# Optimization experiments

Hardware: AMD Instinct MI355X
Metric: run time of the kernel (lower is better)

The kernel has to match this reference:

```python
import jax, jax.numpy as jnp
import numpy as np

B, O, I, D = 8, 128, 128, 1024


def setup_inputs() -> dict:
    key = jax.random.key(0)
    ks = jax.random.split(key, 10)
    s = 1.0 / np.sqrt(2 * D)  # torch Linear default-ish scale
    return {
        "output": jax.random.normal(ks[0], (B, O, D), jnp.float32),
        "context": jax.random.normal(ks[1], (B, I, D), jnp.float32),
        "mask": jax.random.randint(ks[2], (B, I), 0, 2, jnp.int32),
        # self.w = Linear(2*dim, dim), split into the output-half and context-half
        "w_out_w": jax.random.normal(ks[3], (D, D), jnp.float32) * s,
        "w_ctx_w": jax.random.normal(ks[4], (D, D), jnp.float32) * s,
        "w_b": jax.random.normal(ks[5], (D,), jnp.float32) * s,
        # self.score = Linear(dim, 1)
        "score_w": jax.random.normal(ks[6], (D,), jnp.float32) * (1.0 / np.sqrt(D)),
        "score_b": jnp.zeros((), jnp.float32),
        # self.linear_out = Linear(2*dim, dim)
        "lin_w": jax.random.normal(ks[7], (2 * D, D), jnp.float32) * s,
        "lin_b": jax.random.normal(ks[8], (D,), jnp.float32) * s,
    }


def reference(output, context, mask, w_out_w, w_ctx_w, w_b, score_w, score_b, lin_w, lin_b):
    # Additive (Bahdanau) attention.
    # cat(out, ctx) @ W^T == out @ W1 + ctx @ W2  -> avoid [B,O,I,2D] concat.
    s_out = jnp.einsum('bod,de->boe', output, w_out_w)            # [B,O,D]
    s_ctx = jnp.einsum('bid,de->bie', context, w_ctx_w)           # [B,I,D]
    h = jax.nn.leaky_relu(s_out[:, :, None, :] + s_ctx[:, None, :, :] + w_b)  # [B,O,I,D]
    score = jnp.einsum('boid,d->boi', h, score_w) + score_b       # [B,O,I]
    score = jnp.where(mask[:, None, :] == 1, -jnp.inf, score)
    attn = jax.nn.softmax(score, axis=-1)                         # [B,O,I]
    attn_output = jnp.einsum('boi,bid->bod', attn, context)       # mix=True: bmm
    # fn=True: linear_out on cat(attn_output, output) then leaky_relu
    combined = jnp.concatenate([attn_output, output], axis=-1)    # [B,O,2D]
    attn_output = jax.nn.leaky_relu(combined @ lin_w + lin_b)     # [B,O,D]
    return attn_output, attn
```

## Files before the change

kernel.cpp:

```cpp
#include <hip/hip_runtime.h>

namespace {

constexpr int kB = 8, kO = 128, kI = 128, kD = 1024;
constexpr long kOutAttnOff = (long)kB * kO * kD;

typedef __attribute__((ext_vector_type(8))) short short8;
typedef __attribute__((ext_vector_type(4))) float f32x4;

__device__ __forceinline__ float leaky(float x) { return fmaxf(x, 0.01f * x); }

__device__ __forceinline__ short f2bf(float f) {
    unsigned u = __builtin_bit_cast(unsigned, f);
    u += 0x7FFFu + ((u >> 16) & 1u);
    return (short)(u >> 16);
}

__device__ __forceinline__ void gll16(const void* g, void* l) {
    __builtin_amdgcn_global_load_lds(
        (const __attribute__((address_space(1))) int*)g,
        (__attribute__((address_space(3))) int*)l, 16, 0, 0);
}

__global__ __launch_bounds__(256)
void conv_all(const float* __restrict__ output, const float* __restrict__ context,
              const float* __restrict__ w1, const float* __restrict__ w2,
              const float* __restrict__ lin,
              short* __restrict__ ob16, short* __restrict__ cb16,
              short* __restrict__ w1t, short* __restrict__ w2t,
              short* __restrict__ lint)
{
    __shared__ float T[64][68];
    const int bid = blockIdx.x, tid = threadIdx.x;

    if (bid < 1024) {
        const int idx = bid * 256 + tid;
        const float* src; short* dst; int i;
        if (idx < (1 << 17)) { src = output;  dst = ob16; i = idx; }
        else                 { src = context; dst = cb16; i = idx - (1 << 17); }
        const float4* s4 = (const float4*)src + (long)i * 2;
        const float4 v0 = s4[0], v1 = s4[1];
        short8 r;
        r[0] = f2bf(v0.x); r[1] = f2bf(v0.y); r[2] = f2bf(v0.z); r[3] = f2bf(v0.w);
        r[4] = f2bf(v1.x); r[5] = f2bf(v1.y); r[6] = f2bf(v1.z); r[7] = f2bf(v1.w);
        *(short8*)(dst + (long)i * 8) = r;
        return;
    }

    const int tb = bid - 1024;
    const float* src; short* dst; long C, R; int t2;
    if (tb < 256)      { src = w1;  dst = w1t;  R = 1024; C = 1024; t2 = tb; }
    else if (tb < 512) { src = w2;  dst = w2t;  R = 1024; C = 1024; t2 = tb - 256; }
    else               { src = lin; dst = lint; R = 2048; C = 1024; t2 = tb - 512; }
    const int tr = t2 >> 4, tc = t2 & 15;
    const int r = tid >> 2, q = tid & 3;

    const float* s = src + (long)(tr * 64 + r) * C + tc * 64 + q * 16;
    const float4 a0 = ((const float4*)s)[0];
    const float4 a1 = ((const float4*)s)[1];
    const float4 a2 = ((const float4*)s)[2];
    const float4 a3 = ((const float4*)s)[3];
    *(float4*)&T[r][q * 16 + 0]  = a0;
    *(float4*)&T[r][q * 16 + 4]  = a1;
    *(float4*)&T[r][q * 16 + 8]  = a2;
    *(float4*)&T[r][q * 16 + 12] = a3;
    __syncthreads();

    short8 o0, o1;
#pragma unroll
    for (int j = 0; j < 8; ++j)  o0[j] = f2bf(T[q * 16 + j][r]);
#pragma unroll
    for (int j = 0; j < 8; ++j)  o1[j] = f2bf(T[q * 16 + 8 + j][r]);
    short* dp = dst + (long)(tc * 64 + r) * R + tr * 64 + q * 16;
    *(short8*)dp       = o0;
    *((short8*)dp + 1) = o1;
}

__global__ __launch_bounds__(256)
void mm_jobs(const short* __restrict__ ob16, const short* __restrict__ cb16,
             const short* __restrict__ w1t, const short* __restrict__ w2t,
             const short* __restrict__ lint,
             const float* __restrict__ w_b, const float* __restrict__ lin_b,
             float* __restrict__ s_out, float* __restrict__ s_ctx,
             float* __restrict__ outlin, short* __restrict__ ctxlin)
{
    __shared__ short As[2][64][64];
    __shared__ short Bs[2][128][64];
    const int tid = threadIdx.x;
    const int t = blockIdx.x;
    const int lane = tid & 63, w = tid >> 6;

    const short *Ap, *Bp;
    int lda, ldb, bm, bn, ldc;
    const float* bias = nullptr;
    float* Cf = nullptr;
    short* Ch = nullptr;

    if (t < 384) {
        const int job = t >> 7, jt = t & 127;
        bm = (jt >> 3) * 64; bn = (jt & 7) * 128;
        lda = 1024; ldc = 1024;
        if (job == 0)      { Ap = ob16; Bp = w1t;         ldb = 1024; bias = w_b;   Cf = s_out;  }
        else if (job == 1) { Ap = cb16; Bp = w2t;         ldb = 1024;               Cf = s_ctx;  }
        else               { Ap = ob16; Bp = lint + 1024; ldb = 2048; bias = lin_b; Cf = outlin; }
    } else {
        const int tt = t - 384, bz = tt >> 4, tw = tt & 15;
        bm = tw * 64; bn = 0;
        Ap = lint; lda = 2048;
        Bp = cb16 + (long)bz * (kI * kD); ldb = 1024;
        Ch = ctxlin + (long)bz * (kD * kI); ldc = 128;
    }

    const int m0 = (w >> 1) * 32, n0 = (w & 1) * 64;
    const int fr = lane & 15, fcol = lane >> 4, sl = lane & 7;
    const int r8 = lane >> 3;
    const int sw8 = ((lane & 7) ^ r8) * 8;
    const int w16 = w * 16, w32 = w * 32;

    f32x4 acc[2][4] = {};

    auto stage = [&](int buf, int k0) {
        const short* ga = Ap + (long)(bm + w16 + r8) * lda + k0 + sw8;
        gll16(ga,                 &As[buf][w16][0]);
        gll16(ga + 8 * (long)lda, &As[buf][w16 + 8][0]);
        const short* gb = Bp + (long)(bn + w32 + r8) * ldb + k0 + sw8;
        gll16(gb,                  &Bs[buf][w32][0]);
        gll16(gb + 8 * (long)ldb,  &Bs[buf][w32 + 8][0]);
        gll16(gb + 16 * (long)ldb, &Bs[buf][w32 + 16][0]);
        gll16(gb + 24 * (long)ldb, &Bs[buf][w32 + 24][0]);
    };

    stage(0, 0);
    __syncthreads();
    int cur = 0;
    for (int s = 0; s < 16; ++s) {
        if (s < 15) stage(cur ^ 1, (s + 1) << 6);
#pragma unroll
        for (int ks8 = 0; ks8 < 8; ks8 += 4) {
            const int sa = ((ks8 + fcol) ^ sl) * 8;
            short8 a[2], b[4];
#pragma unroll
            for (int mi = 0; mi < 2; ++mi)
                a[mi] = *(const short8*)&As[cur][m0 + mi * 16 + fr][sa];
#pragma unroll
            for (int ni = 0; ni < 4; ++ni)
                b[ni] = *(const short8*)&Bs[cur][n0 + ni * 16 + fr][sa];
#pragma unroll
            for (int mi = 0; mi < 2; ++mi)
#pragma unroll
                for (int ni = 0; ni < 4; ++ni)
                    acc[mi][ni] = __builtin_amdgcn_mfma_f32_16x16x32_bf16(
                        a[mi], b[ni], acc[mi][ni], 0, 0, 0);
        }
        __syncthreads();
        cur ^= 1;
    }

    float bv[4] = {0, 0, 0, 0};
    if (bias) {
#pragma unroll
        for (int ni = 0; ni < 4; ++ni) bv[ni] = bias[bn + n0 + ni * 16 + fr];
    }
#pragma unroll
    for (int mi = 0; mi < 2; ++mi)
#pragma unroll
        for (int ni = 0; ni < 4; ++ni)
#pragma unroll
            for (int r = 0; r < 4; ++r) {
                const int row = bm + m0 + mi * 16 + ((lane >> 4) << 2) + r;
                const int col = bn + n0 + ni * 16 + fr;
                float v = acc[mi][ni][r] + bv[ni];
                if (Ch) Ch[(long)row * ldc + col] = f2bf(v);
                else    Cf[(long)row * ldc + col] = v;
            }
}

__global__ __launch_bounds__(256)
void score_softmax5(const float* __restrict__ s_out, const float* __restrict__ s_ctx,
                    const float* __restrict__ score_w, const float* __restrict__ score_b,
                    const int* __restrict__ mask, float* __restrict__ attn_f32,
                    short* __restrict__ attn_b16)
{
    __shared__ float As[4][1032];
    __shared__ float Cs[2][128][64];
    __shared__ float Wsh[1024];
    __shared__ float Ps[4][4][128];
    __shared__ int   Msk[128];

    const int b   = blockIdx.x;
    const int o0  = blockIdx.y * 4;
    const int tid = threadIdx.x;
    const int wv  = tid >> 6;
    const int ln  = tid & 63;

    const float* arow = s_out + (long)(b * kO + o0) * kD;
#pragma unroll
    for (int q = 0; q < 4; ++q) {
        const int tq = tid + q * 256;
        const int rr = tq >> 8, c4 = (tq & 255) * 4;
        *(float4*)&As[rr][c4] = *(const float4*)&arow[(long)rr * kD + c4];
    }
    *(float4*)&Wsh[tid * 4] = *(const float4*)&score_w[tid * 4];
    if (tid < 128) Msk[tid] = mask[b * kI + tid];

    const float* crow = s_ctx + (long)b * kI * kD;
    const int srow = wv * 4 + (ln >> 4);
    const int cho  = ((ln & 15) ^ (srow & 7)) * 4;

    auto stageCs = [&](int buf, int dc) {
#pragma unroll
        for (int it = 0; it < 8; ++it)
            gll16(crow + (long)(srow + it * 16) * kD + dc + cho,
                  &Cs[buf][wv * 4 + it * 16][0]);
    };

    float a0[4] = {}, a1[4] = {};
    const int kb = wv * 16;

    stageCs(0, 0);
    __syncthreads();
    int buf = 0;
    for (int c = 0; c < 16; ++c) {
        const int dc = c * 64;
        if (c < 15) stageCs(buf ^ 1, dc + 64);
#pragma unroll
        for (int kq = 0; kq < 4; ++kq) {
            const int sc = ((wv * 4 + kq) ^ (ln & 7)) * 4;
            const float4 c0 = *(const float4*)&Cs[buf][ln][sc];
            const float4 c1 = *(const float4*)&Cs[buf][ln + 64][sc];
            const float4 w4 = *(const float4*)&Wsh[dc + kb + kq * 4];
#pragma unroll
            for (int o = 0; o < 4; ++o) {
                const float4 av = *(const float4*)&As[o][dc + kb + kq * 4];
                a0[o] = fmaf(leaky(av.x + c0.x), w4.x, a0[o]);
                a0[o] = fmaf(leaky(av.y + c0.y), w4.y, a0[o]);
                a0[o] = fmaf(leaky(av.z + c0.z), w4.z, a0[o]);
                a0[o] = fmaf(leaky(av.w + c0.w), w4.w, a0[o]);
                a1[o] = fmaf(leaky(av.x + c1.x), w4.x, a1[o]);
                a1[o] = fmaf(leaky(av.y + c1.y), w4.y, a1[o]);
                a1[o] = fmaf(leaky(av.z + c1.z), w4.z, a1[o]);
                a1[o] = fmaf(leaky(av.w + c1.w), w4.w, a1[o]);
            }
        }
        __syncthreads();
        buf ^= 1;
    }

#pragma unroll
    for (int o = 0; o < 4; ++o) {
        Ps[wv][o][ln]      = a0[o];
        Ps[wv][o][ln + 64] = a1[o];
    }
    __syncthreads();

    const int ow = wv;
    const float negInf = -__builtin_huge_valf();
    const float sb = score_b[0];
    float s0 = Ps[0][ow][ln]      + Ps[1][ow][ln]
             + Ps[2][ow][ln]      + Ps[3][ow][ln]      + sb;
    float s1 = Ps[0][ow][ln + 64] + Ps[1][ow][ln + 64]
             + Ps[2][ow][ln + 64] + Ps[3][ow][ln + 64] + sb;
    if (Msk[ln]      != 0) s0 = negInf;
    if (Msk[ln + 64] != 0) s1 = negInf;

    float m = fmaxf(s0, s1);
#pragma unroll
    for (int d = 1; d < 64; d <<= 1) m = fmaxf(m, __shfl_xor(m, d, 64));
    const float e0 = __expf(s0 - m);
    const float e1 = __expf(s1 - m);
    float sum = e0 + e1;
#pragma unroll
    for (int d = 1; d < 64; d <<= 1) sum += __shfl_xor(sum, d, 64);
    const float inv = 1.0f / sum;

    const long rowoff = (long)(b * kO + o0 + ow) * kI;
    float* ro = attn_f32 + rowoff;
    short* rh = attn_b16 + rowoff;
    const float p0 = e0 * inv, p1 = e1 * inv;
    ro[ln]      = p0;
    ro[ln + 64] = p1;
    rh[ln]      = f2bf(p0);
    rh[ln + 64] = f2bf(p1);
}

__global__ __launch_bounds__(256)
void gemm_final(const short* __restrict__ A, const short* __restrict__ Bt,
                const float* __restrict__ addend, float* __restrict__ C)
{
    __shared__ short As[2][64][64];
    __shared__ short Bs[2][64][64];
    const int tid = threadIdx.x;
    const int bn = blockIdx.x * 64, bm = blockIdx.y * 64;
    const long z = blockIdx.z;
    const short* Az = A + z * (long)(kO * kI);
    const short* Bz = Bt + z * (long)(kD * kI);
    const float* adz = addend + z * (long)(kO * kD);
    float* Cz = C + z * (long)(kO * kD);

    const int lane = tid & 63, w = tid >> 6;
    const int w16 = w * 16;
    const int m0 = (w >> 1) * 32, n0 = (w & 1) * 32;
    const int fr = lane & 15, fcol = lane >> 4, sl = lane & 7;
    const int r8 = lane >> 3;
    const int sw8 = ((lane & 7) ^ r8) * 8;

    f32x4 acc[2][2] = {};

    auto stage = [&](int buf, int k0) {
        const short* ga = Az + (long)(bm + w16 + r8) * kI + k0 + sw8;
        gll16(ga,          &As[buf][w16][0]);
        gll16(ga + 8 * kI, &As[buf][w16 + 8][0]);
        const short* gb = Bz + (long)(bn + w16 + r8) * kI + k0 + sw8;
        gll16(gb,          &Bs[buf][w16][0]);
        gll16(gb + 8 * kI, &Bs[buf][w16 + 8][0]);
    };

    stage(0, 0);
    __syncthreads();
    int cur = 0;
    for (int s = 0; s < 2; ++s) {
        if (s == 0) stage(1, 64);
#pragma unroll
        for (int ks8 = 0; ks8 < 8; ks8 += 4) {
            const int sa = ((ks8 + fcol) ^ sl) * 8;
            const short8 a0 = *(const short8*)&As[cur][m0 + fr][sa];
            const short8 a1 = *(const short8*)&As[cur][m0 + 16 + fr][sa];
            const short8 b0 = *(const short8*)&Bs[cur][n0 + fr][sa];
            const short8 b1 = *(const short8*)&Bs[cur][n0 + 16 + fr][sa];
            acc[0][0] = __builtin_amdgcn_mfma_f32_16x16x32_bf16(a0, b0, acc[0][0], 0, 0, 0);
            acc[0][1] = __builtin_amdgcn_mfma_f32_16x16x32_bf16(a0, b1, acc[0][1], 0, 0, 0);
            acc[1][0] = __builtin_amdgcn_mfma_f32_16x16x32_bf16(a1, b0, acc[1][0], 0, 0, 0);
            acc[1][1] = __builtin_amdgcn_mfma_f32_16x16x32_bf16(a1, b1, acc[1][1], 0, 0, 0);
        }
        __syncthreads();
        cur ^= 1;
    }

#pragma unroll
    for (int mi = 0; mi < 2; ++mi)
#pragma unroll
        for (int ni = 0; ni < 2; ++ni)
#pragma unroll
            for (int r = 0; r < 4; ++r) {
                const int row = bm + m0 + mi * 16 + ((lane >> 4) << 2) + r;
                const int col = bn + n0 + ni * 16 + fr;
                const float v = acc[mi][ni][r] + adz[(long)row * kD + col];
                Cz[(long)row * kD + col] = leaky(v);
            }
}

}

extern "C" void kernel_launch(void* const* d_in, const int* in_sizes, int n_in,
                              void* d_out, int out_size, void* d_ws, size_t ws_size,
                              hipStream_t stream)
{
    const float* output  = (const float*)d_in[0];
    const float* context = (const float*)d_in[1];
    const int*   mask    = (const int*)d_in[2];
    const float* w_out_w = (const float*)d_in[3];
    const float* w_ctx_w = (const float*)d_in[4];
    const float* w_b     = (const float*)d_in[5];
    const float* score_w = (const float*)d_in[6];
    const float* score_b = (const float*)d_in[7];
    const float* lin_w   = (const float*)d_in[8];
    const float* lin_b   = (const float*)d_in[9];

    float* out_main = (float*)d_out;
    float* out_attn = out_main + kOutAttnOff;
    float* s_out    = out_main;

    char* wp = (char*)d_ws;
    float* s_ctx  = (float*)wp;  wp += (size_t)4 << 20;
    short* ob16   = (short*)wp;  wp += (size_t)2 << 20;
    short* cb16   = (short*)wp;  wp += (size_t)2 << 20;
    short* w1t    = (short*)wp;  wp += (size_t)2 << 20;
    short* w2t    = (short*)wp;  wp += (size_t)2 << 20;
    short* lint   = (short*)wp;  wp += (size_t)4 << 20;
    float* outlin = (float*)wp;  wp += (size_t)4 << 20;
    short* ctxlin = (short*)wp;  wp += (size_t)2 << 20;
    short* attn16 = (short*)wp;

    const dim3 blk(256);

    hipLaunchKernelGGL(conv_all, dim3(2048), blk, 0, stream,
        output, context, w_out_w, w_ctx_w, lin_w, ob16, cb16, w1t, w2t, lint);

    hipLaunchKernelGGL(mm_jobs, dim3(512), blk, 0, stream,
        ob16, cb16, w1t, w2t, lint, w_b, lin_b, s_out, s_ctx, outlin, ctxlin);

    hipLaunchKernelGGL(score_softmax5, dim3(8, 32), blk, 0, stream,
        s_out, s_ctx, score_w, score_b, mask, out_attn, attn16);

    hipLaunchKernelGGL(gemm_final, dim3(16, 2, 8), blk, 0, stream,
        attn16, ctxlin, outlin, out_main);
}
```

Measured before the change: 68.55 us.

## Fuse all four stages into one cooperative kernel with grid syncs and bf16 intermediates

Replaces the four separate launches (conversion, projection GEMMs, score/softmax, final GEMM) with a single cooperative kernel of 512 blocks that uses grid-wide syncs between phases and one shared-memory buffer reused by every phase. The s_out/s_ctx projections are now stored as bf16 instead of fp32, which halves their traffic in the score phase, and the score phase is remapped to two output rows per block. The aim is to remove launch gaps and shrink intermediate memory traffic. In exchange it adds grid-sync costs, reduces the precision of the score inputs, and each phase is bound to the same fixed 512-block grid, so some phases leave blocks idle.

```diff
diff --git a/kernel.cpp b/kernel.cpp
--- a/kernel.cpp
+++ b/kernel.cpp
@@ -1,4 +1,7 @@
 #include <hip/hip_runtime.h>
+#include <hip/hip_cooperative_groups.h>
+
+namespace cg = cooperative_groups;
 
 namespace {
 
@@ -15,6 +18,9 @@
     u += 0x7FFFu + ((u >> 16) & 1u);
     return (short)(u >> 16);
 }
+__device__ __forceinline__ float bf2f(short h) {
+    return __builtin_bit_cast(float, ((unsigned)(unsigned short)h) << 16);
+}
 
 __device__ __forceinline__ void gll16(const void* g, void* l) {
     __builtin_amdgcn_global_load_lds(
@@ -22,331 +28,326 @@
         (__attribute__((address_space(3))) int*)l, 16, 0, 0);
 }
 
-__global__ __launch_bounds__(256)
-void conv_all(const float* __restrict__ output, const float* __restrict__ context,
-              const float* __restrict__ w1, const float* __restrict__ w2,
-              const float* __restrict__ lin,
-              short* __restrict__ ob16, short* __restrict__ cb16,
-              short* __restrict__ w1t, short* __restrict__ w2t,
-              short* __restrict__ lint)
+struct Params {
+    const float *output, *context; const int* mask;
+    const float *w1, *w2, *w_b, *score_w, *score_b, *lin, *lin_b;
+    float *out_main, *out_attn;
+    short *ob16, *cb16, *w1t, *w2t, *lint;
+    short *s_out16, *s_ctx16; float* outlin; short *ctxlin, *attn16;
+};
+
+__global__ __launch_bounds__(256, 2) void fused(Params p)
 {
-    __shared__ float T[64][68];
+    __shared__ __align__(16) char smem[49152];
+    cg::grid_group grid = cg::this_grid();
     const int bid = blockIdx.x, tid = threadIdx.x;
-
-    if (bid < 1024) {
+    const int lane = tid & 63, wv = tid >> 6;
+
+    {
         const int idx = bid * 256 + tid;
         const float* src; short* dst; int i;
-        if (idx < (1 << 17)) { src = output;  dst = ob16; i = idx; }
-        else                 { src = context; dst = cb16; i = idx - (1 << 17); }
-        const float4* s4 = (const float4*)src + (long)i * 2;
-        const float4 v0 = s4[0], v1 = s4[1];
-        short8 r;
-        r[0] = f2bf(v0.x); r[1] = f2bf(v0.y); r[2] = f2bf(v0.z); r[3] = f2bf(v0.w);
-        r[4] = f2bf(v1.x); r[5] = f2bf(v1.y); r[6] = f2bf(v1.z); r[7] = f2bf(v1.w);
-        *(short8*)(dst + (long)i * 8) = r;
-        return;
-    }
-
-    const int tb = bid - 1024;
-    const float* src; short* dst; long C, R; int t2;
-    if (tb < 256)      { src = w1;  dst = w1t;  R = 1024; C = 1024; t2 = tb; }
-    else if (tb < 512) { src = w2;  dst = w2t;  R = 1024; C = 1024; t2 = tb - 256; }
-    else               { src = lin; dst = lint; R = 2048; C = 1024; t2 = tb - 512; }
-    const int tr = t2 >> 4, tc = t2 & 15;
-    const int r = tid >> 2, q = tid & 3;
-
-    const float* s = src + (long)(tr * 64 + r) * C + tc * 64 + q * 16;
-    const float4 a0 = ((const float4*)s)[0];
-    const float4 a1 = ((const float4*)s)[1];
-    const float4 a2 = ((const float4*)s)[2];
-    const float4 a3 = ((const float4*)s)[3];
-    *(float4*)&T[r][q * 16 + 0]  = a0;
-    *(float4*)&T[r][q * 16 + 4]  = a1;
-    *(float4*)&T[r][q * 16 + 8]  = a2;
-    *(float4*)&T[r][q * 16 + 12] = a3;
-    __syncthreads();
-
-    short8 o0, o1;
-#pragma unroll
-    for (int j = 0; j < 8; ++j)  o0[j] = f2bf(T[q * 16 + j][r]);
-#pragma unroll
-    for (int j = 0; j < 8; ++j)  o1[j] = f2bf(T[q * 16 + 8 + j][r]);
-    short* dp = dst + (long)(tc * 64 + r) * R + tr * 64 + q * 16;
-    *(short8*)dp       = o0;
-    *((short8*)dp + 1) = o1;
-}
-
-__global__ __launch_bounds__(256)
-void mm_jobs(const short* __restrict__ ob16, const short* __restrict__ cb16,
-             const short* __restrict__ w1t, const short* __restrict__ w2t,
-             const short* __restrict__ lint,
-             const float* __restrict__ w_b, const float* __restrict__ lin_b,
-             float* __restrict__ s_out, float* __restrict__ s_ctx,
-             float* __restrict__ outlin, short* __restrict__ ctxlin)
-{
-    __shared__ short As[2][64][64];
-    __shared__ short Bs[2][128][64];
-    const int tid = threadIdx.x;
-    const int t = blockIdx.x;
-    const int lane = tid & 63, w = tid >> 6;
-
-    const short *Ap, *Bp;
-    int lda, ldb, bm, bn, ldc;
-    const float* bias = nullptr;
-    float* Cf = nullptr;
-    short* Ch = nullptr;
-
-    if (t < 384) {
-        const int job = t >> 7, jt = t & 127;
-        bm = (jt >> 3) * 64; bn = (jt & 7) * 128;
-        lda = 1024; ldc = 1024;
-        if (job == 0)      { Ap = ob16; Bp = w1t;         ldb = 1024; bias = w_b;   Cf = s_out;  }
-        else if (job == 1) { Ap = cb16; Bp = w2t;         ldb = 1024;               Cf = s_ctx;  }
-        else               { Ap = ob16; Bp = lint + 1024; ldb = 2048; bias = lin_b; Cf = outlin; }
-    } else {
-        const int tt = t - 384, bz = tt >> 4, tw = tt & 15;
-        bm = tw * 64; bn = 0;
-        Ap = lint; lda = 2048;
-        Bp = cb16 + (long)bz * (kI * kD); ldb = 1024;
-        Ch = ctxlin + (long)bz * (kD * kI); ldc = 128;
-    }
-
-    const int m0 = (w >> 1) * 32, n0 = (w & 1) * 64;
-    const int fr = lane & 15, fcol = lane >> 4, sl = lane & 7;
-    const int r8 = lane >> 3;
-    const int sw8 = ((lane & 7) ^ r8) * 8;
-    const int w16 = w * 16, w32 = w * 32;
-
-    f32x4 acc[2][4] = {};
-
-    auto stage = [&](int buf, int k0) {
-        const short* ga = Ap + (long)(bm + w16 + r8) * lda + k0 + sw8;
-        gll16(ga,                 &As[buf][w16][0]);
-        gll16(ga + 8 * (long)lda, &As[buf][w16 + 8][0]);
-        const short* gb = Bp + (long)(bn + w32 + r8) * ldb + k0 + sw8;
-        gll16(gb,                  &Bs[buf][w32][0]);
-        gll16(gb + 8 * (long)ldb,  &Bs[buf][w32 + 8][0]);
-        gll16(gb + 16 * (long)ldb, &Bs[buf][w32 + 16][0]);
-        gll16(gb + 24 * (long)ldb, &Bs[buf][w32 + 24][0]);
-    };
-
-    stage(0, 0);
-    __syncthreads();
-    int cur = 0;
-    for (int s = 0; s < 16; ++s) {
-        if (s < 15) stage(cur ^ 1, (s + 1) << 6);
-#pragma unroll
-        for (int ks8 = 0; ks8 < 8; ks8 += 4) {
-            const int sa = ((ks8 + fcol) ^ sl) * 8;
-            short8 a[2], b[4];
-#pragma unroll
-            for (int mi = 0; mi < 2; ++mi)
-                a[mi] = *(const short8*)&As[cur][m0 + mi * 16 + fr][sa];
+        if (idx < 65536) { src = p.output;  dst = p.ob16; i = idx; }
+        else             { src = p.context; dst = p.cb16; i = idx - 65536; }
+        const float4* s4 = (const float4*)src + (long)i * 4;
+        const float4 v0 = s4[0], v1 = s4[1], v2 = s4[2], v3 = s4[3];
+        short8 r0, r1;
+        r0[0]=f2bf(v0.x); r0[1]=f2bf(v0.y); r0[2]=f2bf(v0.z); r0[3]=f2bf(v0.w);
+        r0[4]=f2bf(v1.x); r0[5]=f2bf(v1.y); r0[6]=f2bf(v1.z); r0[7]=f2bf(v1.w);
+        r1[0]=f2bf(v2.x); r1[1]=f2bf(v2.y); r1[2]=f2bf(v2.z); r1[3]=f2bf(v2.w);
+        r1[4]=f2bf(v3.x); r1[5]=f2bf(v3.y); r1[6]=f2bf(v3.z); r1[7]=f2bf(v3.w);
+        short8* d8 = (short8*)(dst + (long)i * 16);
+        d8[0] = r0; d8[1] = r1;
+    }
+    {
+        float (*T)[68] = reinterpret_cast<float(*)[68]>(smem);
+        const int r = tid >> 2, q = tid & 3;
+        for (int j = 0; j < 2; ++j) {
+            const int tj = bid * 2 + j;
+            const float* src; short* dst; long C, R; int t2;
+            if (tj < 256)      { src = p.w1;  dst = p.w1t;  R = 1024; C = 1024; t2 = tj; }
+            else if (tj < 512) { src = p.w2;  dst = p.w2t;  R = 1024; C = 1024; t2 = tj - 256; }
+            else               { src = p.lin; dst = p.lint; R = 2048; C = 1024; t2 = tj - 512; }
+            const int tr = t2 >> 4, tc = t2 & 15;
+            const float* s = src + (long)(tr * 64 + r) * C + tc * 64 + q * 16;
+            const float4 a0 = ((const float4*)s)[0];
+            const float4 a1 = ((const float4*)s)[1];
+            const float4 a2 = ((const float4*)s)[2];
+            const float4 a3 = ((const float4*)s)[3];
+            __syncthreads();
+            *(float4*)&T[r][q * 16 + 0]  = a0;
+            *(float4*)&T[r][q * 16 + 4]  = a1;
+            *(float4*)&T[r][q * 16 + 8]  = a2;
+            *(float4*)&T[r][q * 16 + 12] = a3;
+            __syncthreads();
+            short8 o0, o1;
+#pragma unroll
+            for (int jj = 0; jj < 8; ++jj) o0[jj] = f2bf(T[q * 16 + jj][r]);
+#pragma unroll
+            for (int jj = 0; jj < 8; ++jj) o1[jj] = f2bf(T[q * 16 + 8 + jj][r]);
+            short* dp = dst + (long)(tc * 64 + r) * R + tr * 64 + q * 16;
+            *(short8*)dp       = o0;
+            *((short8*)dp + 1) = o1;
+        }
+    }
+    grid.sync();
+
+    {
+        short (*As)[64] = reinterpret_cast<short(*)[64]>(smem);
+        short (*Bs)[64] = reinterpret_cast<short(*)[64]>(smem + 16384);
+        const int t = bid;
+        const short *Ap, *Bp;
+        int lda, ldb, bm, bn, ldc;
+        const float* bias = nullptr;
+        float* Cf = nullptr; short* Ch = nullptr;
+
+        if (t < 384) {
+            const int job = t >> 7, jt = t & 127;
+            bm = (jt >> 3) * 64; bn = (jt & 7) * 128; lda = 1024; ldc = 1024;
+            if (job == 0)      { Ap = p.ob16; Bp = p.w1t;         ldb = 1024; bias = p.w_b;   Ch = p.s_out16; }
+            else if (job == 1) { Ap = p.cb16; Bp = p.w2t;         ldb = 1024;                 Ch = p.s_ctx16; }
+            else               { Ap = p.ob16; Bp = p.lint + 1024; ldb = 2048; bias = p.lin_b; Cf = p.outlin;  }
+        } else {
+            const int tt = t - 384, bz = tt >> 4, tw = tt & 15;
+            bm = tw * 64; bn = 0;
+            Ap = p.lint; lda = 2048;
+            Bp = p.cb16 + (long)bz * (kI * kD); ldb = 1024;
+            Ch = p.ctxlin + (long)bz * (kD * kI); ldc = 128;
+        }
+
+        const int m0 = (wv >> 1) * 32, n0 = (wv & 1) * 64;
+        const int fr = lane & 15, fcol = lane >> 4, sl = lane & 7, r8 = lane >> 3;
+        const int sw8 = ((lane & 7) ^ r8) * 8;
+        const int w16 = wv * 16, w32 = wv * 32;
+
+        f32x4 acc[2][4] = {};
+        auto stage = [&](int buf, int k0) {
+            const short* ga = Ap + (long)(bm + w16 + r8) * lda + k0 + sw8;
+            gll16(ga,                 &As[buf * 64 + w16][0]);
+            gll16(ga + 8 * (long)lda, &As[buf * 64 + w16 + 8][0]);
+            const short* gb = Bp + (long)(bn + w32 + r8) * ldb + k0 + sw8;
+            gll16(gb,                  &Bs[buf * 128 + w32][0]);
+            gll16(gb + 8 * (long)ldb,  &Bs[buf * 128 + w32 + 8][0]);
+            gll16(gb + 16 * (long)ldb, &Bs[buf * 128 + w32 + 16][0]);
+            gll16(gb + 24 * (long)ldb, &Bs[buf * 128 + w32 + 24][0]);
+        };
+
+        stage(0, 0);
+        __syncthreads();
+        int cur = 0;
+        for (int s = 0; s < 16; ++s) {
+            if (s < 15) stage(cur ^ 1, (s + 1) << 6);
+#pragma unroll
+            for (int ks8 = 0; ks8 < 8; ks8 += 4) {
+                const int sa = ((ks8 + fcol) ^ sl) * 8;
+                short8 a[2], b[4];
+#pragma unroll
+                for (int mi = 0; mi < 2; ++mi)
+                    a[mi] = *(const short8*)&As[cur * 64 + m0 + mi * 16 + fr][sa];
+#pragma unroll
+                for (int ni = 0; ni < 4; ++ni)
+                    b[ni] = *(const short8*)&Bs[cur * 128 + n0 + ni * 16 + fr][sa];
+#pragma unroll
+                for (int mi = 0; mi < 2; ++mi)
+#pragma unroll
+                    for (int ni = 0; ni < 4; ++ni)
+                        acc[mi][ni] = __builtin_amdgcn_mfma_f32_16x16x32_bf16(
+                            a[mi], b[ni], acc[mi][ni], 0, 0, 0);
+            }
+            __syncthreads();
+            cur ^= 1;
+        }
+
+        float bv[4] = {0, 0, 0, 0};
+        if (bias) {
+#pragma unroll
+            for (int ni = 0; ni < 4; ++ni) bv[ni] = bias[bn + n0 + ni * 16 + fr];
+        }
+#pragma unroll
+        for (int mi = 0; mi < 2; ++mi)
 #pragma unroll
             for (int ni = 0; ni < 4; ++ni)
-                b[ni] = *(const short8*)&Bs[cur][n0 + ni * 16 + fr][sa];
-#pragma unroll
-            for (int mi = 0; mi < 2; ++mi)
-#pragma unroll
-                for (int ni = 0; ni < 4; ++ni)
-                    acc[mi][ni] = __builtin_amdgcn_mfma_f32_16x16x32_bf16(
-                        a[mi], b[ni], acc[mi][ni], 0, 0, 0);
-        }
+#pragma unroll
+                for (int r = 0; r < 4; ++r) {
+                    const int row = bm + m0 + mi * 16 + ((lane >> 4) << 2) + r;
+                    const int col = bn + n0 + ni * 16 + fr;
+                    const float v = acc[mi][ni][r] + bv[ni];
+                    if (Ch) Ch[(long)row * ldc + col] = f2bf(v);
+                    else    Cf[(long)row * ldc + col] = v;
+                }
+    }
+    grid.sync();
+
+    {
+        short (*Cs)[64] = reinterpret_cast<short(*)[64]>(smem);
+        short* As2 = reinterpret_cast<short*>(smem + 32768);
+        float* Wsh = reinterpret_cast<float*>(smem + 36864);
+        float* Ps  = reinterpret_cast<float*>(smem + 40960);
+        int*   Msk = reinterpret_cast<int*>(smem + 45056);
+
+        const int b = bid >> 6, o0 = (bid & 63) * 2;
+        const int ln = lane;
+        {
+            const int r = tid >> 7, c8 = tid & 127;
+            *(short8*)(As2 + r * 1024 + c8 * 8) =
+                *(const short8*)(p.s_out16 + (long)(b * kO + o0 + r) * kD + c8 * 8);
+        }
+        *(float4*)&Wsh[tid * 4] = *(const float4*)&p.score_w[tid * 4];
+        if (tid < 128) Msk[tid] = p.mask[b * kI + tid];
+
+        const int kb = wv * 16;
+        auto stageCs = [&](int buf, int dc) {
+#pragma unroll
+            for (int it = 0; it < 4; ++it) {
+                const int base = wv * 32 + it * 8;
+                const int rr = base + (lane >> 3);
+                const int c16 = (lane & 7) ^ (rr & 7);
+                gll16(p.s_ctx16 + (long)(b * kI + rr) * kD + dc + c16 * 8,
+                      &Cs[buf * 128 + base][0]);
+            }
+        };
+
+        float a00 = 0, a01 = 0, a10 = 0, a11 = 0;
+        stageCs(0, 0);
         __syncthreads();
-        cur ^= 1;
-    }
-
-    float bv[4] = {0, 0, 0, 0};
-    if (bias) {
-#pragma unroll
-        for (int ni = 0; ni < 4; ++ni) bv[ni] = bias[bn + n0 + ni * 16 + fr];
-    }
-#pragma unroll
-    for (int mi = 0; mi < 2; ++mi)
-#pragma unroll
-        for (int ni = 0; ni < 4; ++ni)
-#pragma unroll
-            for (int r = 0; r < 4; ++r) {
-                const int row = bm + m0 + mi * 16 + ((lane >> 4) << 2) + r;
-                const int col = bn + n0 + ni * 16 + fr;
-                float v = acc[mi][ni][r] + bv[ni];
-                if (Ch) Ch[(long)row * ldc + col] = f2bf(v);
-                else    Cf[(long)row * ldc + col] = v;
-            }
-}
-
-__global__ __launch_bounds__(256)
-void score_softmax5(const float* __restrict__ s_out, const float* __restrict__ s_ctx,
-                    const float* __restrict__ score_w, const float* __restrict__ score_b,
-                    const int* __restrict__ mask, float* __restrict__ attn_f32,
-                    short* __restrict__ attn_b16)
-{
-    __shared__ float As[4][1032];
-    __shared__ float Cs[2][128][64];
-    __shared__ float Wsh[1024];
-    __shared__ float Ps[4][4][128];
-    __shared__ int   Msk[128];
-
-    const int b   = blockIdx.x;
-    const int o0  = blockIdx.y * 4;
-    const int tid = threadIdx.x;
-    const int wv  = tid >> 6;
-    const int ln  = tid & 63;
-
-    const float* arow = s_out + (long)(b * kO + o0) * kD;
-#pragma unroll
-    for (int q = 0; q < 4; ++q) {
-        const int tq = tid + q * 256;
-        const int rr = tq >> 8, c4 = (tq & 255) * 4;
-        *(float4*)&As[rr][c4] = *(const float4*)&arow[(long)rr * kD + c4];
-    }
-    *(float4*)&Wsh[tid * 4] = *(const float4*)&score_w[tid * 4];
-    if (tid < 128) Msk[tid] = mask[b * kI + tid];
-
-    const float* crow = s_ctx + (long)b * kI * kD;
-    const int srow = wv * 4 + (ln >> 4);
-    const int cho  = ((ln & 15) ^ (srow & 7)) * 4;
-
-    auto stageCs = [&](int buf, int dc) {
-#pragma unroll
-        for (int it = 0; it < 8; ++it)
-            gll16(crow + (long)(srow + it * 16) * kD + dc + cho,
-                  &Cs[buf][wv * 4 + it * 16][0]);
-    };
-
-    float a0[4] = {}, a1[4] = {};
-    const int kb = wv * 16;
-
-    stageCs(0, 0);
-    __syncthreads();
-    int buf = 0;
-    for (int c = 0; c < 16; ++c) {
-        const int dc = c * 64;
-        if (c < 15) stageCs(buf ^ 1, dc + 64);
-#pragma unroll
-        for (int kq = 0; kq < 4; ++kq) {
-            const int sc = ((wv * 4 + kq) ^ (ln & 7)) * 4;
-            const float4 c0 = *(const float4*)&Cs[buf][ln][sc];
-            const float4 c1 = *(const float4*)&Cs[buf][ln + 64][sc];
-            const float4 w4 = *(const float4*)&Wsh[dc + kb + kq * 4];
-#pragma unroll
-            for (int o = 0; o < 4; ++o) {
-                const float4 av = *(const float4*)&As[o][dc + kb + kq * 4];
-                a0[o] = fmaf(leaky(av.x + c0.x), w4.x, a0[o]);
-                a0[o] = fmaf(leaky(av.y + c0.y), w4.y, a0[o]);
-                a0[o] = fmaf(leaky(av.z + c0.z), w4.z, a0[o]);
-                a0[o] = fmaf(leaky(av.w + c0.w), w4.w, a0[o]);
-                a1[o] = fmaf(leaky(av.x + c1.x), w4.x, a1[o]);
-                a1[o] = fmaf(leaky(av.y + c1.y), w4.y, a1[o]);
-                a1[o] = fmaf(leaky(av.z + c1.z), w4.z, a1[o]);
-                a1[o] = fmaf(leaky(av.w + c1.w), w4.w, a1[o]);
-            }
-        }
+        int buf = 0;
+        for (int c = 0; c < 16; ++c) {
+            const int dc = c * 64;
+            if (c < 15) stageCs(buf ^ 1, dc + 64);
+            float wr[16], av0[16], av1[16];
+            {
+                const short8 x0 = *(const short8*)(As2 + dc + kb);
+                const short8 x1 = *(const short8*)(As2 + dc + kb + 8);
+                const short8 y0 = *(const short8*)(As2 + 1024 + dc + kb);
+                const short8 y1 = *(const short8*)(As2 + 1024 + dc + kb + 8);
+#pragma unroll
+                for (int d = 0; d < 8; ++d) {
+                    av0[d] = bf2f(x0[d]); av0[d + 8] = bf2f(x1[d]);
+                    av1[d] = bf2f(y0[d]); av1[d + 8] = bf2f(y1[d]);
+                }
+#pragma unroll
+                for (int q = 0; q < 4; ++q) {
+                    const float4 ww = *(const float4*)&Wsh[dc + kb + q * 4];
+                    wr[q*4] = ww.x; wr[q*4+1] = ww.y; wr[q*4+2] = ww.z; wr[q*4+3] = ww.w;
+                }
+            }
+#pragma unroll
+            for (int h = 0; h < 2; ++h) {
+                const int i = ln + h * 64;
+                const int sA = (((wv << 1) | 0) ^ (i & 7)) * 8;
+                const int sB = (((wv << 1) | 1) ^ (i & 7)) * 8;
+                const short8 cA = *(const short8*)&Cs[buf * 128 + i][sA];
+                const short8 cB = *(const short8*)&Cs[buf * 128 + i][sB];
+                float cf[16];
+#pragma unroll
+                for (int d = 0; d < 8; ++d) { cf[d] = bf2f(cA[d]); cf[d + 8] = bf2f(cB[d]); }
+                float s0 = 0, s1 = 0;
+#pragma unroll
+                for (int d = 0; d < 16; ++d) {
+                    s0 = fmaf(leaky(av0[d] + cf[d]), wr[d], s0);
+                    s1 = fmaf(leaky(av1[d] + cf[d]), wr[d], s1);
+                }
+                if (h == 0) { a00 += s0; a10 += s1; }
+                else        { a01 += s0; a11 += s1; }
+            }
+            __syncthreads();
+            buf ^= 1;
+        }
+
+        Ps[(wv * 2 + 0) * 128 + ln]      = a00;
+        Ps[(wv * 2 + 0) * 128 + ln + 64] = a01;
+        Ps[(wv * 2 + 1) * 128 + ln]      = a10;
+        Ps[(wv * 2 + 1) * 128 + ln + 64] = a11;
         __syncthreads();
-        buf ^= 1;
-    }
-
-#pragma unroll
-    for (int o = 0; o < 4; ++o) {
-        Ps[wv][o][ln]      = a0[o];
-        Ps[wv][o][ln + 64] = a1[o];
-    }
-    __syncthreads();
-
-    const int ow = wv;
-    const float negInf = -__builtin_huge_valf();
-    const float sb = score_b[0];
-    float s0 = Ps[0][ow][ln]      + Ps[1][ow][ln]
-             + Ps[2][ow][ln]      + Ps[3][ow][ln]      + sb;
-    float s1 = Ps[0][ow][ln + 64] + Ps[1][ow][ln + 64]
-             + Ps[2][ow][ln + 64] + Ps[3][ow][ln + 64] + sb;
-    if (Msk[ln]      != 0) s0 = negInf;
-    if (Msk[ln + 64] != 0) s1 = negInf;
-
-    float m = fmaxf(s0, s1);
-#pragma unroll
-    for (int d = 1; d < 64; d <<= 1) m = fmaxf(m, __shfl_xor(m, d, 64));
-    const float e0 = __expf(s0 - m);
-    const float e1 = __expf(s1 - m);
-    float sum = e0 + e1;
-#pragma unroll
-    for (int d = 1; d < 64; d <<= 1) sum += __shfl_xor(sum, d, 64);
-    const float inv = 1.0f / sum;
-
-    const long rowoff = (long)(b * kO + o0 + ow) * kI;
-    float* ro = attn_f32 + rowoff;
-    short* rh = attn_b16 + rowoff;
-    const float p0 = e0 * inv, p1 = e1 * inv;
-    ro[ln]      = p0;
-    ro[ln + 64] = p1;
-    rh[ln]      = f2bf(p0);
-    rh[ln + 64] = f2bf(p1);
-}
-
-__global__ __launch_bounds__(256)
-void gemm_final(const short* __restrict__ A, const short* __restrict__ Bt,
-                const float* __restrict__ addend, float* __restrict__ C)
-{
-    __shared__ short As[2][64][64];
-    __shared__ short Bs[2][64][64];
-    const int tid = threadIdx.x;
-    const int bn = blockIdx.x * 64, bm = blockIdx.y * 64;
-    const long z = blockIdx.z;
-    const short* Az = A + z * (long)(kO * kI);
-    const short* Bz = Bt + z * (long)(kD * kI);
-    const float* adz = addend + z * (long)(kO * kD);
-    float* Cz = C + z * (long)(kO * kD);
-
-    const int lane = tid & 63, w = tid >> 6;
-    const int w16 = w * 16;
-    const int m0 = (w >> 1) * 32, n0 = (w & 1) * 32;
-    const int fr = lane & 15, fcol = lane >> 4, sl = lane & 7;
-    const int r8 = lane >> 3;
-    const int sw8 = ((lane & 7) ^ r8) * 8;
-
-    f32x4 acc[2][2] = {};
-
-    auto stage = [&](int buf, int k0) {
-        const short* ga = Az + (long)(bm + w16 + r8) * kI + k0 + sw8;
-        gll16(ga,          &As[buf][w16][0]);
-        gll16(ga + 8 * kI, &As[buf][w16 + 8][0]);
-        const short* gb = Bz + (long)(bn + w16 + r8) * kI + k0 + sw8;
-        gll16(gb,          &Bs[buf][w16][0]);
-        gll16(gb + 8 * kI, &Bs[buf][w16 + 8][0]);
-    };
-
-    stage(0, 0);
-    __syncthreads();
-    int cur = 0;
-    for (int s = 0; s < 2; ++s) {
-        if (s == 0) stage(1, 64);
-#pragma unroll
-        for (int ks8 = 0; ks8 < 8; ks8 += 4) {
-            const int sa = ((ks8 + fcol) ^ sl) * 8;
-            const short8 a0 = *(const short8*)&As[cur][m0 + fr][sa];
-            const short8 a1 = *(const short8*)&As[cur][m0 + 16 + fr][sa];
-            const short8 b0 = *(const short8*)&Bs[cur][n0 + fr][sa];
-            const short8 b1 = *(const short8*)&Bs[cur][n0 + 16 + fr][sa];
-            acc[0][0] = __builtin_amdgcn_mfma_f32_16x16x32_bf16(a0, b0, acc[0][0], 0, 0, 0);
-            acc[0][1] = __builtin_amdgcn_mfma_f32_16x16x32_bf16(a0, b1, acc[0][1], 0, 0, 0);
-            acc[1][0] = __builtin_amdgcn_mfma_f32_16x16x32_bf16(a1, b0, acc[1][0], 0, 0, 0);
-            acc[1][1] = __builtin_amdgcn_mfma_f32_16x16x32_bf16(a1, b1, acc[1][1], 0, 0, 0);
-        }
+
+        if (wv < 2) {
+            const int ow = wv;
+            const float negInf = -__builtin_huge_valf();
+            const float sb = p.score_b[0];
+            float s0 = Ps[(0 + ow) * 128 + ln]       + Ps[(2 + ow) * 128 + ln]
+                     + Ps[(4 + ow) * 128 + ln]       + Ps[(6 + ow) * 128 + ln]       + sb;
+            float s1 = Ps[(0 + ow) * 128 + ln + 64]  + Ps[(2 + ow) * 128 + ln + 64]
+                     + Ps[(4 + ow) * 128 + ln + 64]  + Ps[(6 + ow) * 128 + ln + 64]  + sb;
+            if (Msk[ln]      != 0) s0 = negInf;
+            if (Msk[ln + 64] != 0) s1 = negInf;
+
+            float m = fmaxf(s0, s1);
+#pragma unroll
+            for (int d = 1; d < 64; d <<= 1) m = fmaxf(m, __shfl_xor(m, d, 64));
+            const float e0 = __expf(s0 - m);
+            const float e1 = __expf(s1 - m);
+            float sum = e0 + e1;
+#pragma unroll
+            for (int d = 1; d < 64; d <<= 1) sum += __shfl_xor(sum, d, 64);
+            const float inv = 1.0f / sum;
+
+            const long rowoff = (long)(b * kO + o0 + ow) * kI;
+            const float p0 = e0 * inv, p1 = e1 * inv;
+            p.out_attn[rowoff + ln]      = p0;
+            p.out_attn[rowoff + ln + 64] = p1;
+            p.attn16[rowoff + ln]        = f2bf(p0);
+            p.attn16[rowoff + ln + 64]   = f2bf(p1);
+        }
+    }
+    grid.sync();
+
+    if (bid < 256) {
+        short (*As)[64] = reinterpret_cast<short(*)[64]>(smem);
+        short (*Bs)[64] = reinterpret_cast<short(*)[64]>(smem + 16384);
+        const int z = bid >> 5, tile = bid & 31;
+        const int bm = (tile >> 4) * 64, bn = (tile & 15) * 64;
+        const short* Az = p.attn16 + (long)z * (kO * kI);
+        const short* Bz = p.ctxlin + (long)z * (kD * kI);
+        const float* adz = p.outlin + (long)z * (kO * kD);
+        float* Cz = p.out_main + (long)z * (kO * kD);
+
+        const int m0 = (wv >> 1) * 32, n0 = (wv & 1) * 32;
+        const int fr = lane & 15, fcol = lane >> 4, sl = lane & 7, r8 = lane >> 3;
+        const int sw8 = ((lane & 7) ^ r8) * 8;
+        const int w16 = wv * 16;
+
+        f32x4 acc[2][2] = {};
+        auto stage = [&](int buf, int k0) {
+            const short* ga = Az + (long)(bm + w16 + r8) * kI + k0 + sw8;
+            gll16(ga,          &As[buf * 64 + w16][0]);
+            gll16(ga + 8 * kI, &As[buf * 64 + w16 + 8][0]);
+            const short* gb = Bz + (long)(bn + w16 + r8) * kI + k0 + sw8;
+            gll16(gb,          &Bs[buf * 64 + w16][0]);
+            gll16(gb + 8 * kI, &Bs[buf * 64 + w16 + 8][0]);
+        };
+
+        stage(0, 0);
         __syncthreads();
-        cur ^= 1;
-    }
-
-#pragma unroll
-    for (int mi = 0; mi < 2; ++mi)
-#pragma unroll
-        for (int ni = 0; ni < 2; ++ni)
-#pragma unroll
-            for (int r = 0; r < 4; ++r) {
-                const int row = bm + m0 + mi * 16 + ((lane >> 4) << 2) + r;
-                const int col = bn + n0 + ni * 16 + fr;
-                const float v = acc[mi][ni][r] + adz[(long)row * kD + col];
-                Cz[(long)row * kD + col] = leaky(v);
-            }
+        int cur = 0;
+        for (int s = 0; s < 2; ++s) {
+            if (s == 0) stage(1, 64);
+#pragma unroll
+            for (int ks8 = 0; ks8 < 8; ks8 += 4) {
+                const int sa = ((ks8 + fcol) ^ sl) * 8;
+                const short8 a0 = *(const short8*)&As[cur * 64 + m0 + fr][sa];
+                const short8 a1 = *(const short8*)&As[cur * 64 + m0 + 16 + fr][sa];
+                const short8 b0 = *(const short8*)&Bs[cur * 64 + n0 + fr][sa];
+                const short8 b1 = *(const short8*)&Bs[cur * 64 + n0 + 16 + fr][sa];
+                acc[0][0] = __builtin_amdgcn_mfma_f32_16x16x32_bf16(a0, b0, acc[0][0], 0, 0, 0);
+                acc[0][1] = __builtin_amdgcn_mfma_f32_16x16x32_bf16(a0, b1, acc[0][1], 0, 0, 0);
+                acc[1][0] = __builtin_amdgcn_mfma_f32_16x16x32_bf16(a1, b0, acc[1][0], 0, 0, 0);
+                acc[1][1] = __builtin_amdgcn_mfma_f32_16x16x32_bf16(a1, b1, acc[1][1], 0, 0, 0);
+            }
+            __syncthreads();
+            cur ^= 1;
+        }
+
+#pragma unroll
+        for (int mi = 0; mi < 2; ++mi)
+#pragma unroll
+            for (int ni = 0; ni < 2; ++ni)
+#pragma unroll
+                for (int r = 0; r < 4; ++r) {
+                    const int row = bm + m0 + mi * 16 + ((lane >> 4) << 2) + r;
+                    const int col = bn + n0 + ni * 16 + fr;
+                    Cz[(long)row * kD + col] =
+                        leaky(acc[mi][ni][r] + adz[(long)row * kD + col]);
+                }
+    }
 }
 
 }
@@ -368,30 +369,30 @@
 
     float* out_main = (float*)d_out;
     float* out_attn = out_main + kOutAttnOff;
-    float* s_out    = out_main;
 
     char* wp = (char*)d_ws;
-    float* s_ctx  = (float*)wp;  wp += (size_t)4 << 20;
-    short* ob16   = (short*)wp;  wp += (size_t)2 << 20;
-    short* cb16   = (short*)wp;  wp += (size_t)2 << 20;
-    short* w1t    = (short*)wp;  wp += (size_t)2 << 20;
-    short* w2t    = (short*)wp;  wp += (size_t)2 << 20;
-    short* lint   = (short*)wp;  wp += (size_t)4 << 20;
-    float* outlin = (float*)wp;  wp += (size_t)4 << 20;
-    short* ctxlin = (short*)wp;  wp += (size_t)2 << 20;
-    short* attn16 = (short*)wp;
-
-    const dim3 blk(256);
-
-    hipLaunchKernelGGL(conv_all, dim3(2048), blk, 0, stream,
-        output, context, w_out_w, w_ctx_w, lin_w, ob16, cb16, w1t, w2t, lint);
-
-    hipLaunchKernelGGL(mm_jobs, dim3(512), blk, 0, stream,
-        ob16, cb16, w1t, w2t, lint, w_b, lin_b, s_out, s_ctx, outlin, ctxlin);
-
-    hipLaunchKernelGGL(score_softmax5, dim3(8, 32), blk, 0, stream,
-        s_out, s_ctx, score_w, score_b, mask, out_attn, attn16);
-
-    hipLaunchKernelGGL(gemm_final, dim3(16, 2, 8), blk, 0, stream,
-        attn16, ctxlin, outlin, out_main);
-}
+    short* ob16    = (short*)wp;  wp += (size_t)2 << 20;
+    short* cb16    = (short*)wp;  wp += (size_t)2 << 20;
+    short* w1t     = (short*)wp;  wp += (size_t)2 << 20;
+    short* w2t     = (short*)wp;  wp += (size_t)2 << 20;
+    short* lint    = (short*)wp;  wp += (size_t)4 << 20;
+    short* s_out16 = (short*)wp;  wp += (size_t)2 << 20;
+    short* s_ctx16 = (short*)wp;  wp += (size_t)2 << 20;
+    float* outlin  = (float*)wp;  wp += (size_t)4 << 20;
+    short* ctxlin  = (short*)wp;  wp += (size_t)2 << 20;
+    short* attn16  = (short*)wp;
+
+    Params prm;
+    prm.output = output; prm.context = context; prm.mask = mask;
+    prm.w1 = w_out_w; prm.w2 = w_ctx_w; prm.w_b = w_b;
+    prm.score_w = score_w; prm.score_b = score_b;
+    prm.lin = lin_w; prm.lin_b = lin_b;
+    prm.out_main = out_main; prm.out_attn = out_attn;
+    prm.ob16 = ob16; prm.cb16 = cb16; prm.w1t = w1t; prm.w2t = w2t; prm.lint = lint;
+    prm.s_out16 = s_out16; prm.s_ctx16 = s_ctx16; prm.outlin = outlin;
+    prm.ctxlin = ctxlin; prm.attn16 = attn16;
+
+    void* args[] = { &prm };
+    hipLaunchCooperativeKernel((const void*)fused, dim3(512), dim3(256),
+                               args, 0, stream);
+}
```

Result: slower. 243.4 us (+255.1%).
